# Performance work log

Hardware: AMD Instinct MI355X
Metric: run time of the kernel (lower is better)

The kernel has to match this reference:

```python
import jax, jax.numpy as jnp
import numpy as np

B, L1, Q_DIM, V_DIM = 4, 4096, 256, 256
NH, NL, NP = 8, 4, 4
LEVELS = [(128, 128), (64, 64), (32, 32), (16, 16)]
L2 = sum(h * w for h, w in LEVELS)  # 21760


def setup_inputs() -> dict:
    key = jax.random.key(0)
    ks = jax.random.split(key, 12)
    xav = lambda k, so, si: jax.random.normal(k, (so, si), jnp.float32) * np.sqrt(2.0 / (so + si)).astype(np.float32)
    # reference windows: centers in [0.1,0.9], box sizes in [0.05,0.25]
    c = 0.1 + 0.8 * jax.random.uniform(ks[0], (B, L1, 2), jnp.float32)
    s = 0.05 + 0.2 * jax.random.uniform(ks[1], (B, L1, 2), jnp.float32)
    v_shape = jnp.array(LEVELS, dtype=jnp.int32)
    v_start_index = jnp.array(np.cumsum([0] + [h * w for h, w in LEVELS[:-1]]), dtype=jnp.int32)
    return {
        'query': jax.random.normal(ks[2], (B, L1, Q_DIM), jnp.float32),
        'value': jax.random.normal(ks[3], (B, L2, V_DIM), jnp.float32),
        'v_shape': v_shape,
        'v_mask': jnp.zeros((B, L2), jnp.bool_),
        'v_start_index': v_start_index,
        'v_valid_ratios': jnp.ones((B, 1, 1, NL, 1, 2), jnp.float32),
        'ref_windows': jnp.concatenate([c, s], axis=-1),
        'Wo': 0.01 * jax.random.normal(ks[4], (NH * NL * NP * 2, Q_DIM), jnp.float32),
        'bo': 0.5 * jax.random.normal(ks[5], (NH * NL * NP * 2,), jnp.float32),
        'Wa': 0.02 * jax.random.normal(ks[6], (NH * NL * NP, Q_DIM), jnp.float32),
        'ba': jnp.zeros((NH * NL * NP,), jnp.float32),
        'Wv': xav(ks[7], V_DIM, V_DIM),
        'bv': jnp.zeros((V_DIM,), jnp.float32),
        'Wout': xav(ks[8], Q_DIM, V_DIM),
        'bout': jnp.zeros((Q_DIM,), jnp.float32),
    }


def _ms_deform_sample(value, v_shape, v_start, loc):
    """value: (b,l2,h,d); loc: (b,l1,h,L,P,2) in [0,1] -> (b,l1,L,P,h,d).
    Bilinear sampling with zero padding, align_corners=False semantics."""
    b, l2, h, d = value.shape
    _, l1, _, L, P, _ = loc.shape
    Hi = v_shape[:, 0][None, None, None, :, None]  # (1,1,1,L,1) int
    Wi = v_shape[:, 1][None, None, None, :, None]
    x = loc[..., 0] * Wi.astype(loc.dtype) - 0.5  # (b,l1,h,L,P)
    y = loc[..., 1] * Hi.astype(loc.dtype) - 0.5
    x0 = jnp.floor(x)
    y0 = jnp.floor(y)
    lx, ly = x - x0, y - y0
    x0i = x0.astype(jnp.int32)
    y0i = y0.astype(jnp.int32)
    start = v_start[None, None, None, :, None]
    acc = jnp.zeros((b, l1 * L * P, h, d), loc.dtype)
    for dy, wy in ((0, 1.0 - ly), (1, ly)):
        for dx, wx in ((0, 1.0 - lx), (1, lx)):
            xi = x0i + dx
            yi = y0i + dy
            valid = (xi >= 0) & (xi < Wi) & (yi >= 0) & (yi < Hi)
            w = wx * wy * valid.astype(loc.dtype)  # (b,l1,h,L,P)
            xc = jnp.clip(xi, 0, Wi - 1)
            yc = jnp.clip(yi, 0, Hi - 1)
            flat = start + yc * Wi + xc  # (b,l1,h,L,P) index into l2
            flat_t = flat.transpose(0, 1, 3, 4, 2).reshape(b, l1 * L * P, h)
            w_t = w.transpose(0, 1, 3, 4, 2).reshape(b, l1 * L * P, h)
            g = jnp.take_along_axis(value, flat_t[..., None], axis=1)  # (b,M,h,d)
            acc = acc + g * w_t[..., None]
    return acc.reshape(b, l1, L, P, h, d)


def reference(query, value, v_shape, v_mask, v_start_index, v_valid_ratios, ref_windows,
              Wo, bo, Wa, ba, Wv, bv, Wout, bout):
    b, l1, _ = query.shape
    l2 = value.shape[1]
    hd = value.shape[-1] // NH
    v = value @ Wv.T + bv
    v = jnp.where(v_mask[..., None], 0.0, v).reshape(b, l2, NH, hd)
    off = (query @ Wo.T + bo).reshape(b, l1, NH, NL, NP, 2)
    attn = jax.nn.softmax((query @ Wa.T + ba).reshape(b, l1, NH, NL * NP), axis=-1)
    attn = attn.reshape(b, l1, NH, NL, NP)
    loc = ref_windows[:, :, None, None, None, :2] + off / 8.0 * ref_windows[:, :, None, None, None, 2:]
    loc = loc * v_valid_ratios
    sampled = _ms_deform_sample(v, v_shape, v_start_index, loc)  # (b,l1,L,P,h,d)
    out = jnp.einsum('blLPhd,blhLP->blhd', sampled, attn).reshape(b, l1, NH * hd)
    out = out @ Wout.T + bout
    return out, attn
```

## Files before the change

kernel.cpp:

```cpp
#include <hip/hip_runtime.h>
#include <cstdint>
#include <cstddef>


#define L2_LEN 21760
#define BQ_TOT 16384

typedef __attribute__((ext_vector_type(8))) _Float16 half8;
typedef __attribute__((ext_vector_type(4))) _Float16 half4;
typedef __attribute__((ext_vector_type(2))) _Float16 half2v;
typedef __attribute__((ext_vector_type(4))) float    f32x4;

__device__ __forceinline__ void glds16(const _Float16* g, _Float16* l) {
    __builtin_amdgcn_global_load_lds(
        (const __attribute__((address_space(1))) void*)g,
        (__attribute__((address_space(3))) void*)l, 16, 0, 0);
}
__device__ __forceinline__ half8 cvt8(float4 a, float4 b) {
    half8 h;
    h[0] = (_Float16)a.x; h[1] = (_Float16)a.y;
    h[2] = (_Float16)a.z; h[3] = (_Float16)a.w;
    h[4] = (_Float16)b.x; h[5] = (_Float16)b.y;
    h[6] = (_Float16)b.z; h[7] = (_Float16)b.w;
    return h;
}
__device__ __forceinline__ int swz_chunk(int c) {
    const int frag = c >> 6, r = (c >> 2) & 15, k = c & 3;
    return (frag * 64 + ((k * 16 + r) ^ (k << 2))) * 8;
}

__global__ __launch_bounds__(256, 3) void gemm_vproj(
    const float* __restrict__ A, const float* __restrict__ Wv,
    const float* __restrict__ bv, const unsigned char* __restrict__ mask,
    _Float16* __restrict__ vh)
{
    __shared__ _Float16 As[2][4096];
    __shared__ _Float16 Bs[2][4096];

    const int t = threadIdx.x, lane = t & 63, wid = t >> 6;
    const int wm = wid >> 1, wn = wid & 1;
    const int bm = blockIdx.x, bn = blockIdx.y;

    const int r0 = t >> 2, kg = (t & 3) * 8;
    const float* Ag0 = A  + ((size_t)(bm * 128) + r0) * 256 + kg;
    const float* Ag1 = Ag0 + (size_t)64 * 256;
    const float* Bg0 = Wv + ((size_t)(bn * 128) + r0) * 256 + kg;
    const float* Bg1 = Bg0 + (size_t)64 * 256;
    const int d0 = swz_chunk(t), d1 = swz_chunk(t + 256);
    const int rsw = (lane ^ ((lane >> 4) << 2)) * 8;

    f32x4 acc[4][4] = {};
    float4 pa0, pa1, pa2, pa3, pb0, pb1, pb2, pb3;

    pa0 = *(const float4*)Ag0; pa1 = *(const float4*)(Ag0 + 4);
    pa2 = *(const float4*)Ag1; pa3 = *(const float4*)(Ag1 + 4);
    pb0 = *(const float4*)Bg0; pb1 = *(const float4*)(Bg0 + 4);
    pb2 = *(const float4*)Bg1; pb3 = *(const float4*)(Bg1 + 4);
    *(half8*)&As[0][d0] = cvt8(pa0, pa1); *(half8*)&As[0][d1] = cvt8(pa2, pa3);
    *(half8*)&Bs[0][d0] = cvt8(pb0, pb1); *(half8*)&Bs[0][d1] = cvt8(pb2, pb3);
    __syncthreads();

    for (int it = 0; it < 8; ++it) {
        const int cur = it & 1;
        if (it < 7) {
            const int kk = (it + 1) * 32;
            pa0 = *(const float4*)(Ag0 + kk); pa1 = *(const float4*)(Ag0 + kk + 4);
            pa2 = *(const float4*)(Ag1 + kk); pa3 = *(const float4*)(Ag1 + kk + 4);
            pb0 = *(const float4*)(Bg0 + kk); pb1 = *(const float4*)(Bg0 + kk + 4);
            pb2 = *(const float4*)(Bg1 + kk); pb3 = *(const float4*)(Bg1 + kk + 4);
        }
        half8 ah[4], bh[4];
#pragma unroll
        for (int x = 0; x < 4; ++x) {
            ah[x] = *(const half8*)&As[cur][(wm * 4 + x) * 512 + rsw];
            bh[x] = *(const half8*)&Bs[cur][(wn * 4 + x) * 512 + rsw];
        }
#pragma unroll
        for (int m = 0; m < 4; ++m)
#pragma unroll
            for (int n = 0; n < 4; ++n)
                acc[m][n] = __builtin_amdgcn_mfma_f32_16x16x32_f16(
                    bh[n], ah[m], acc[m][n], 0, 0, 0);
        if (it < 7) {
            *(half8*)&As[cur ^ 1][d0] = cvt8(pa0, pa1);
            *(half8*)&As[cur ^ 1][d1] = cvt8(pa2, pa3);
            *(half8*)&Bs[cur ^ 1][d0] = cvt8(pb0, pb1);
            *(half8*)&Bs[cur ^ 1][d1] = cvt8(pb2, pb3);
        }
        __syncthreads();
    }

    const int cl = lane & 15, rl = (lane >> 4) * 4;
    const int b = bm / 170;
#pragma unroll
    for (int m = 0; m < 4; ++m) {
        const int row = bm * 128 + wm * 64 + m * 16 + cl;
        const float mz = mask[row] ? 0.0f : 1.0f;
        const int l2i = row - b * L2_LEN;
#pragma unroll
        for (int n = 0; n < 4; ++n) {
            const int col = bn * 128 + wn * 64 + n * 16 + rl;
            const float4 bb = *(const float4*)(bv + col);
            const int h = col >> 5, c = col & 31;
            half4 o;
            o[0] = (_Float16)((acc[m][n][0] + bb.x) * mz);
            o[1] = (_Float16)((acc[m][n][1] + bb.y) * mz);
            o[2] = (_Float16)((acc[m][n][2] + bb.z) * mz);
            o[3] = (_Float16)((acc[m][n][3] + bb.w) * mz);
            *(half4*)(vh + ((size_t)(b * 8 + h) * L2_LEN + l2i) * 32 + c) = o;
        }
    }
}

template<bool A_F16>
__global__ __launch_bounds__(256, 3) void gemm_qo(
    const void* __restrict__ Av,
    const float* __restrict__ W0, const float* __restrict__ W1,
    const float* __restrict__ b0, const float* __restrict__ b1, int n_split,
    float* __restrict__ C, int ldC)
{
    __shared__ _Float16 As[2][4096];
    __shared__ _Float16 Bs[2][4096];

    const int t = threadIdx.x, lane = t & 63, wid = t >> 6;
    const int wm = wid >> 1, wn = wid & 1;
    const int bm = blockIdx.x, bn = blockIdx.y;

    const int cb = bn * 128;
    const float* Wt; const float* bt;
    if (cb < n_split) { Wt = W0 + (size_t)cb * 256;             bt = b0 + cb; }
    else              { Wt = W1 + (size_t)(cb - n_split) * 256; bt = b1 + (cb - n_split); }

    const int r0 = t >> 2, kg = (t & 3) * 8;
    const float* Bg0 = Wt + ((size_t)r0) * 256 + kg;
    const float* Bg1 = Bg0 + (size_t)64 * 256;
    const int d0 = swz_chunk(t), d1 = swz_chunk(t + 256);
    const int rsw = (lane ^ ((lane >> 4) << 2)) * 8;

    const float* Agf0 = nullptr; const float* Agf1 = nullptr;
    const _Float16* Agh0 = nullptr; const _Float16* Agh1 = nullptr;
    _Float16* AdH0 = nullptr; _Float16* AdH1 = nullptr;
    if (A_F16) {
        const int u0 = wid * 128 + lane, u1 = u0 + 64;
        const int ar0 = ((u0 >> 6) << 4) + (u0 & 15), ak0 = ((u0 >> 4) & 3) * 8;
        const int ar1 = ((u1 >> 6) << 4) + (u1 & 15), ak1 = ((u1 >> 4) & 3) * 8;
        Agh0 = (const _Float16*)Av + ((size_t)(bm * 128) + ar0) * 256 + ak0;
        Agh1 = (const _Float16*)Av + ((size_t)(bm * 128) + ar1) * 256 + ak1;
        AdH0 = (_Float16*)&As[0][0] + wid * 1024;
        AdH1 = AdH0 + 512;
    } else {
        Agf0 = (const float*)Av + ((size_t)(bm * 128) + r0) * 256 + kg;
        Agf1 = Agf0 + (size_t)64 * 256;
    }

    f32x4 acc[4][4] = {};
    float4 pa0, pa1, pa2, pa3, pb0, pb1, pb2, pb3;

    pb0 = *(const float4*)Bg0; pb1 = *(const float4*)(Bg0 + 4);
    pb2 = *(const float4*)Bg1; pb3 = *(const float4*)(Bg1 + 4);
    if (A_F16) { glds16(Agh0, AdH0); glds16(Agh1, AdH1); }
    else {
        pa0 = *(const float4*)Agf0; pa1 = *(const float4*)(Agf0 + 4);
        pa2 = *(const float4*)Agf1; pa3 = *(const float4*)(Agf1 + 4);
        *(half8*)&As[0][d0] = cvt8(pa0, pa1);
        *(half8*)&As[0][d1] = cvt8(pa2, pa3);
    }
    *(half8*)&Bs[0][d0] = cvt8(pb0, pb1);
    *(half8*)&Bs[0][d1] = cvt8(pb2, pb3);
    __syncthreads();

    for (int it = 0; it < 8; ++it) {
        const int cur = it & 1;
        if (it < 7) {
            const int kk = (it + 1) * 32;
            if (A_F16) {
                glds16(Agh0 + kk, AdH0 + (cur ^ 1) * 4096);
                glds16(Agh1 + kk, AdH1 + (cur ^ 1) * 4096);
            } else {
                pa0 = *(const float4*)(Agf0 + kk); pa1 = *(const float4*)(Agf0 + kk + 4);
                pa2 = *(const float4*)(Agf1 + kk); pa3 = *(const float4*)(Agf1 + kk + 4);
            }
            pb0 = *(const float4*)(Bg0 + kk); pb1 = *(const float4*)(Bg0 + kk + 4);
            pb2 = *(const float4*)(Bg1 + kk); pb3 = *(const float4*)(Bg1 + kk + 4);
        }
        half8 ah[4], bh[4];
#pragma unroll
        for (int x = 0; x < 4; ++x) {
            ah[x] = *(const half8*)&As[cur][(wm * 4 + x) * 512 + (A_F16 ? lane * 8 : rsw)];
            bh[x] = *(const half8*)&Bs[cur][(wn * 4 + x) * 512 + rsw];
        }
#pragma unroll
        for (int m = 0; m < 4; ++m)
#pragma unroll
            for (int n = 0; n < 4; ++n)
                acc[m][n] = __builtin_amdgcn_mfma_f32_16x16x32_f16(
                    bh[n], ah[m], acc[m][n], 0, 0, 0);
        if (it < 7) {
            if (!A_F16) {
                *(half8*)&As[cur ^ 1][d0] = cvt8(pa0, pa1);
                *(half8*)&As[cur ^ 1][d1] = cvt8(pa2, pa3);
            }
            *(half8*)&Bs[cur ^ 1][d0] = cvt8(pb0, pb1);
            *(half8*)&Bs[cur ^ 1][d1] = cvt8(pb2, pb3);
        }
        __syncthreads();
    }

    const int cl = lane & 15, rl = (lane >> 4) * 4;
#pragma unroll
    for (int m = 0; m < 4; ++m) {
        const int row = bm * 128 + wm * 64 + m * 16 + cl;
#pragma unroll
        for (int n = 0; n < 4; ++n) {
            const int co = wn * 64 + n * 16 + rl;
            const float4 bb = *(const float4*)(bt + co);
            float4 r;
            r.x = acc[m][n][0] + bb.x; r.y = acc[m][n][1] + bb.y;
            r.z = acc[m][n][2] + bb.z; r.w = acc[m][n][3] + bb.w;
            *(float4*)(C + (size_t)row * ldC + cb + co) = r;
        }
    }
}

__global__ __launch_bounds__(128) void sample_fused(
    const _Float16* __restrict__ v,
    const float* __restrict__ qp,
    const float* __restrict__ ref,
    const float* __restrict__ vrp,
    float* __restrict__ attn_out,
    _Float16* __restrict__ sout)
{
    const int t  = threadIdx.x;
    const int q  = blockIdx.x * 4 + (t >> 5);
    const int h  = (t >> 2) & 7;
    const int lv = t & 3;
    const int b  = q >> 12;

    const float* lg = qp + (size_t)q * 384 + 256 + h * 16;
    const float4 l0 = ((const float4*)lg)[0], l1 = ((const float4*)lg)[1];
    const float4 l2 = ((const float4*)lg)[2], l3 = ((const float4*)lg)[3];
    float e[16] = {l0.x, l0.y, l0.z, l0.w, l1.x, l1.y, l1.z, l1.w,
                   l2.x, l2.y, l2.z, l2.w, l3.x, l3.y, l3.z, l3.w};
    float mx = e[0];
#pragma unroll
    for (int j = 1; j < 16; ++j) mx = fmaxf(mx, e[j]);
    float sum = 0.0f;
#pragma unroll
    for (int j = 0; j < 16; ++j) { e[j] = __expf(e[j] - mx); sum += e[j]; }
    const float inv = 1.0f / sum;
    float aw[4];
#pragma unroll
    for (int p = 0; p < 4; ++p) aw[p] = e[lv * 4 + p] * inv;
    *(float4*)(attn_out + ((size_t)q * 8 + h) * 16 + lv * 4) =
        make_float4(aw[0], aw[1], aw[2], aw[3]);

    const float4 rw = *(const float4*)(ref + (size_t)q * 4);
    const float* op = qp + (size_t)q * 384 + h * 32 + lv * 8;
    const float4 o01 = ((const float4*)op)[0], o23 = ((const float4*)op)[1];
    const float oxv[4] = {o01.x, o01.z, o23.x, o23.z};
    const float oyv[4] = {o01.y, o01.w, o23.y, o23.w};

    const int HW = 128 >> lv;
    constexpr int SS[4] = {0, 16384, 20480, 21504};
    const int start = SS[0] * 0 + (lv == 0 ? 0 : (lv == 1 ? 16384 : (lv == 2 ? 20480 : 21504)));
    const float fHW = (float)HW;
    const float vrx = vrp[(b * 4 + lv) * 2 + 0];
    const float vry = vrp[(b * 4 + lv) * 2 + 1];
    const _Float16* vb = v + ((size_t)(b * 8 + h) * L2_LEN + start) * 32;

    float acc[32] = {};

#pragma unroll
    for (int p = 0; p < 4; ++p) {
        const float a = aw[p];
        const float x = (rw.x + oxv[p] * 0.125f * rw.z) * vrx * fHW - 0.5f;
        const float y = (rw.y + oyv[p] * 0.125f * rw.w) * vry * fHW - 0.5f;
        const float x0f = floorf(x), y0f = floorf(y);
        const float fx = x - x0f, fy = y - y0f;
        const int x0 = (int)x0f, y0 = (int)y0f;
        const float wx0 = (x0 >= 0 && x0 < HW)         ? (1.0f - fx) : 0.0f;
        const float wx1 = (x0 + 1 >= 0 && x0 + 1 < HW) ? fx          : 0.0f;
        const float wy0 = (y0 >= 0 && y0 < HW)         ? (1.0f - fy) : 0.0f;
        const float wy1 = (y0 + 1 >= 0 && y0 + 1 < HW) ? fy          : 0.0f;
        const int xc0 = min(max(x0, 0), HW - 1), xc1 = min(max(x0 + 1, 0), HW - 1);
        const int yc0 = min(max(y0, 0), HW - 1), yc1 = min(max(y0 + 1, 0), HW - 1);
        half2v wA, wB;
        wA[0] = (_Float16)(wx0 * wy0 * a); wA[1] = (_Float16)(wx1 * wy0 * a);
        wB[0] = (_Float16)(wx0 * wy1 * a); wB[1] = (_Float16)(wx1 * wy1 * a);

        const uint4* p00 = (const uint4*)(vb + (size_t)(yc0 * HW + xc0) * 32);
        const uint4* p01 = (const uint4*)(vb + (size_t)(yc0 * HW + xc1) * 32);
        const uint4* p10 = (const uint4*)(vb + (size_t)(yc1 * HW + xc0) * 32);
        const uint4* p11 = (const uint4*)(vb + (size_t)(yc1 * HW + xc1) * 32);
        unsigned u00[16], u01[16], u10[16], u11[16];
#pragma unroll
        for (int i = 0; i < 4; ++i) {
            *(uint4*)&u00[i * 4] = p00[i];
            *(uint4*)&u01[i * 4] = p01[i];
            *(uint4*)&u10[i * 4] = p10[i];
            *(uint4*)&u11[i * 4] = p11[i];
        }
#pragma unroll
        for (int d = 0; d < 16; ++d) {
            const unsigned loA = __builtin_amdgcn_perm(u00[d], u01[d], 0x01000504u);
            const unsigned hiA = __builtin_amdgcn_perm(u00[d], u01[d], 0x03020706u);
            const unsigned loB = __builtin_amdgcn_perm(u10[d], u11[d], 0x01000504u);
            const unsigned hiB = __builtin_amdgcn_perm(u10[d], u11[d], 0x03020706u);
#if __has_builtin(__builtin_amdgcn_fdot2)
            acc[2 * d]     = __builtin_amdgcn_fdot2(__builtin_bit_cast(half2v, loA), wA, acc[2 * d], false);
            acc[2 * d]     = __builtin_amdgcn_fdot2(__builtin_bit_cast(half2v, loB), wB, acc[2 * d], false);
            acc[2 * d + 1] = __builtin_amdgcn_fdot2(__builtin_bit_cast(half2v, hiA), wA, acc[2 * d + 1], false);
            acc[2 * d + 1] = __builtin_amdgcn_fdot2(__builtin_bit_cast(half2v, hiB), wB, acc[2 * d + 1], false);
#else
            const half2v xA = __builtin_bit_cast(half2v, loA), yA = __builtin_bit_cast(half2v, hiA);
            const half2v xB = __builtin_bit_cast(half2v, loB), yB = __builtin_bit_cast(half2v, hiB);
            acc[2 * d]     += (float)xA[0] * (float)wA[0] + (float)xA[1] * (float)wA[1]
                            + (float)xB[0] * (float)wB[0] + (float)xB[1] * (float)wB[1];
            acc[2 * d + 1] += (float)yA[0] * (float)wA[0] + (float)yA[1] * (float)wA[1]
                            + (float)yB[0] * (float)wB[0] + (float)yB[1] * (float)wB[1];
#endif
        }
    }

    float t1[32];
#pragma unroll
    for (int j = 0; j < 32; ++j) t1[j] = __shfl_xor(acc[j], 1);
    float r16[16];
#pragma unroll
    for (int j = 0; j < 16; ++j)
        r16[j] = (lv & 1) ? (acc[16 + j] + t1[16 + j]) : (acc[j] + t1[j]);
    float t2[16];
#pragma unroll
    for (int j = 0; j < 16; ++j) t2[j] = __shfl_xor(r16[j], 2);
    float r8[8];
#pragma unroll
    for (int j = 0; j < 8; ++j)
        r8[j] = (lv & 2) ? (r16[8 + j] + t2[8 + j]) : (r16[j] + t2[j]);

    const int cq = ((lv & 1) << 4) | ((lv & 2) << 2);
    half8 o;
#pragma unroll
    for (int j = 0; j < 8; ++j) o[j] = (_Float16)r8[j];
    *(half8*)(sout + (size_t)q * 256 + h * 32 + cq) = o;
}

extern "C" void kernel_launch(void* const* d_in, const int* in_sizes, int n_in,
                              void* d_out, int out_size, void* d_ws, size_t ws_size,
                              hipStream_t stream)
{
    const float*         query    = (const float*)d_in[0];
    const float*         value    = (const float*)d_in[1];
    const unsigned char* v_mask   = (const unsigned char*)d_in[3];
    const float*         v_ratios = (const float*)d_in[5];
    const float*         ref_w    = (const float*)d_in[6];
    const float*         Wo       = (const float*)d_in[7];
    const float*         bo       = (const float*)d_in[8];
    const float*         Wa       = (const float*)d_in[9];
    const float*         ba       = (const float*)d_in[10];
    const float*         Wv       = (const float*)d_in[11];
    const float*         bv       = (const float*)d_in[12];
    const float*         Wout     = (const float*)d_in[13];
    const float*         bout     = (const float*)d_in[14];

    float* out      = (float*)d_out;
    float* attn_out = out + (size_t)BQ_TOT * 256;

    float*    qp = (float*)d_ws;
    _Float16* vh = (_Float16*)(qp + (size_t)BQ_TOT * 384);
    _Float16* Sf = vh + (size_t)4 * L2_LEN * 256;

    gemm_vproj<<<dim3(680, 2), 256, 0, stream>>>(value, Wv, bv, v_mask, vh);
    gemm_qo<false><<<dim3(128, 3), 256, 0, stream>>>(
        query, Wo, Wa, bo, ba, 256, qp, 384);
    sample_fused<<<4096, 128, 0, stream>>>(vh, qp, ref_w, v_ratios, attn_out, Sf);
    gemm_qo<true><<<dim3(128, 2), 256, 0, stream>>>(
        Sf, Wout, Wout, bout, bout, 256, out, 256);
}
```

Baseline: 309.9 us.

## Widen vproj tile to full N and split sampling lanes by channel

```diff
diff --git a/kernel.cpp b/kernel.cpp
--- a/kernel.cpp
+++ b/kernel.cpp
@@ -29,43 +29,41 @@
     return (frag * 64 + ((k * 16 + r) ^ (k << 2))) * 8;
 }
 
-__global__ __launch_bounds__(256, 3) void gemm_vproj(
+__global__ __launch_bounds__(512) void gemm_vproj(
     const float* __restrict__ A, const float* __restrict__ Wv,
     const float* __restrict__ bv, const unsigned char* __restrict__ mask,
     _Float16* __restrict__ vh)
 {
     __shared__ _Float16 As[2][4096];
-    __shared__ _Float16 Bs[2][4096];
+    __shared__ _Float16 Bs[2][8192];
 
     const int t = threadIdx.x, lane = t & 63, wid = t >> 6;
-    const int wm = wid >> 1, wn = wid & 1;
-    const int bm = blockIdx.x, bn = blockIdx.y;
-
-    const int r0 = t >> 2, kg = (t & 3) * 8;
-    const float* Ag0 = A  + ((size_t)(bm * 128) + r0) * 256 + kg;
-    const float* Ag1 = Ag0 + (size_t)64 * 256;
-    const float* Bg0 = Wv + ((size_t)(bn * 128) + r0) * 256 + kg;
-    const float* Bg1 = Bg0 + (size_t)64 * 256;
-    const int d0 = swz_chunk(t), d1 = swz_chunk(t + 256);
+    const int wm = wid >> 2, wn = wid & 3;
+    const int bm = blockIdx.x;
+
+    const float* Ag = A + ((size_t)(bm * 128) + (t >> 2)) * 256 + (t & 3) * 8;
+    const int da = swz_chunk(t);
+    const float* Bg0 = Wv + ((size_t)(t >> 2)) * 256 + (t & 3) * 8;
+    const float* Bg1 = Bg0 + (size_t)128 * 256;
+    const int db0 = swz_chunk(t), db1 = swz_chunk(t + 512);
     const int rsw = (lane ^ ((lane >> 4) << 2)) * 8;
 
     f32x4 acc[4][4] = {};
-    float4 pa0, pa1, pa2, pa3, pb0, pb1, pb2, pb3;
-
-    pa0 = *(const float4*)Ag0; pa1 = *(const float4*)(Ag0 + 4);
-    pa2 = *(const float4*)Ag1; pa3 = *(const float4*)(Ag1 + 4);
+    float4 pa0, pa1, pb0, pb1, pb2, pb3;
+
+    pa0 = *(const float4*)Ag;  pa1 = *(const float4*)(Ag + 4);
     pb0 = *(const float4*)Bg0; pb1 = *(const float4*)(Bg0 + 4);
     pb2 = *(const float4*)Bg1; pb3 = *(const float4*)(Bg1 + 4);
-    *(half8*)&As[0][d0] = cvt8(pa0, pa1); *(half8*)&As[0][d1] = cvt8(pa2, pa3);
-    *(half8*)&Bs[0][d0] = cvt8(pb0, pb1); *(half8*)&Bs[0][d1] = cvt8(pb2, pb3);
+    *(half8*)&As[0][da]  = cvt8(pa0, pa1);
+    *(half8*)&Bs[0][db0] = cvt8(pb0, pb1);
+    *(half8*)&Bs[0][db1] = cvt8(pb2, pb3);
     __syncthreads();
 
     for (int it = 0; it < 8; ++it) {
         const int cur = it & 1;
         if (it < 7) {
             const int kk = (it + 1) * 32;
-            pa0 = *(const float4*)(Ag0 + kk); pa1 = *(const float4*)(Ag0 + kk + 4);
-            pa2 = *(const float4*)(Ag1 + kk); pa3 = *(const float4*)(Ag1 + kk + 4);
+            pa0 = *(const float4*)(Ag + kk);  pa1 = *(const float4*)(Ag + kk + 4);
             pb0 = *(const float4*)(Bg0 + kk); pb1 = *(const float4*)(Bg0 + kk + 4);
             pb2 = *(const float4*)(Bg1 + kk); pb3 = *(const float4*)(Bg1 + kk + 4);
         }
@@ -82,10 +80,9 @@
                 acc[m][n] = __builtin_amdgcn_mfma_f32_16x16x32_f16(
                     bh[n], ah[m], acc[m][n], 0, 0, 0);
         if (it < 7) {
-            *(half8*)&As[cur ^ 1][d0] = cvt8(pa0, pa1);
-            *(half8*)&As[cur ^ 1][d1] = cvt8(pa2, pa3);
-            *(half8*)&Bs[cur ^ 1][d0] = cvt8(pb0, pb1);
-            *(half8*)&Bs[cur ^ 1][d1] = cvt8(pb2, pb3);
+            *(half8*)&As[cur ^ 1][da]  = cvt8(pa0, pa1);
+            *(half8*)&Bs[cur ^ 1][db0] = cvt8(pb0, pb1);
+            *(half8*)&Bs[cur ^ 1][db1] = cvt8(pb2, pb3);
         }
         __syncthreads();
     }
@@ -99,7 +96,7 @@
         const int l2i = row - b * L2_LEN;
 #pragma unroll
         for (int n = 0; n < 4; ++n) {
-            const int col = bn * 128 + wn * 64 + n * 16 + rl;
+            const int col = wn * 64 + n * 16 + rl;
             const float4 bb = *(const float4*)(bv + col);
             const int h = col >> 5, c = col & 31;
             half4 o;
@@ -233,115 +230,103 @@
     const int t  = threadIdx.x;
     const int q  = blockIdx.x * 4 + (t >> 5);
     const int h  = (t >> 2) & 7;
-    const int lv = t & 3;
+    const int c0 = (t & 3) * 8;
     const int b  = q >> 12;
 
     const float* lg = qp + (size_t)q * 384 + 256 + h * 16;
     const float4 l0 = ((const float4*)lg)[0], l1 = ((const float4*)lg)[1];
     const float4 l2 = ((const float4*)lg)[2], l3 = ((const float4*)lg)[3];
-    float e[16] = {l0.x, l0.y, l0.z, l0.w, l1.x, l1.y, l1.z, l1.w,
-                   l2.x, l2.y, l2.z, l2.w, l3.x, l3.y, l3.z, l3.w};
-    float mx = e[0];
-#pragma unroll
-    for (int j = 1; j < 16; ++j) mx = fmaxf(mx, e[j]);
+    float aw[16] = {l0.x, l0.y, l0.z, l0.w, l1.x, l1.y, l1.z, l1.w,
+                    l2.x, l2.y, l2.z, l2.w, l3.x, l3.y, l3.z, l3.w};
+    float mx = aw[0];
+#pragma unroll
+    for (int j = 1; j < 16; ++j) mx = fmaxf(mx, aw[j]);
     float sum = 0.0f;
 #pragma unroll
-    for (int j = 0; j < 16; ++j) { e[j] = __expf(e[j] - mx); sum += e[j]; }
+    for (int j = 0; j < 16; ++j) { aw[j] = __expf(aw[j] - mx); sum += aw[j]; }
     const float inv = 1.0f / sum;
-    float aw[4];
-#pragma unroll
-    for (int p = 0; p < 4; ++p) aw[p] = e[lv * 4 + p] * inv;
-    *(float4*)(attn_out + ((size_t)q * 8 + h) * 16 + lv * 4) =
-        make_float4(aw[0], aw[1], aw[2], aw[3]);
-
+#pragma unroll
+    for (int j = 0; j < 16; ++j) aw[j] *= inv;
+    if (c0 == 0) {
+        float4* ao = (float4*)(attn_out + ((size_t)q * 8 + h) * 16);
+        ao[0] = make_float4(aw[0], aw[1], aw[2], aw[3]);
+        ao[1] = make_float4(aw[4], aw[5], aw[6], aw[7]);
+        ao[2] = make_float4(aw[8], aw[9], aw[10], aw[11]);
+        ao[3] = make_float4(aw[12], aw[13], aw[14], aw[15]);
+    }
+
+    const float* op = qp + (size_t)q * 384 + h * 32;
+    float4 of[8];
+#pragma unroll
+    for (int i = 0; i < 8; ++i) of[i] = ((const float4*)op)[i];
     const float4 rw = *(const float4*)(ref + (size_t)q * 4);
-    const float* op = qp + (size_t)q * 384 + h * 32 + lv * 8;
-    const float4 o01 = ((const float4*)op)[0], o23 = ((const float4*)op)[1];
-    const float oxv[4] = {o01.x, o01.z, o23.x, o23.z};
-    const float oyv[4] = {o01.y, o01.w, o23.y, o23.w};
-
-    const int HW = 128 >> lv;
+    const float4 vr01 = ((const float4*)(vrp + b * 8))[0];
+    const float4 vr23 = ((const float4*)(vrp + b * 8))[1];
+
+    const _Float16* vbase = v + ((size_t)(b * 8 + h) * L2_LEN) * 32 + c0;
     constexpr int SS[4] = {0, 16384, 20480, 21504};
-    const int start = SS[0] * 0 + (lv == 0 ? 0 : (lv == 1 ? 16384 : (lv == 2 ? 20480 : 21504)));
-    const float fHW = (float)HW;
-    const float vrx = vrp[(b * 4 + lv) * 2 + 0];
-    const float vry = vrp[(b * 4 + lv) * 2 + 1];
-    const _Float16* vb = v + ((size_t)(b * 8 + h) * L2_LEN + start) * 32;
-
-    float acc[32] = {};
-
-#pragma unroll
-    for (int p = 0; p < 4; ++p) {
-        const float a = aw[p];
-        const float x = (rw.x + oxv[p] * 0.125f * rw.z) * vrx * fHW - 0.5f;
-        const float y = (rw.y + oyv[p] * 0.125f * rw.w) * vry * fHW - 0.5f;
-        const float x0f = floorf(x), y0f = floorf(y);
-        const float fx = x - x0f, fy = y - y0f;
-        const int x0 = (int)x0f, y0 = (int)y0f;
-        const float wx0 = (x0 >= 0 && x0 < HW)         ? (1.0f - fx) : 0.0f;
-        const float wx1 = (x0 + 1 >= 0 && x0 + 1 < HW) ? fx          : 0.0f;
-        const float wy0 = (y0 >= 0 && y0 < HW)         ? (1.0f - fy) : 0.0f;
-        const float wy1 = (y0 + 1 >= 0 && y0 + 1 < HW) ? fy          : 0.0f;
-        const int xc0 = min(max(x0, 0), HW - 1), xc1 = min(max(x0 + 1, 0), HW - 1);
-        const int yc0 = min(max(y0, 0), HW - 1), yc1 = min(max(y0 + 1, 0), HW - 1);
-        half2v wA, wB;
-        wA[0] = (_Float16)(wx0 * wy0 * a); wA[1] = (_Float16)(wx1 * wy0 * a);
-        wB[0] = (_Float16)(wx0 * wy1 * a); wB[1] = (_Float16)(wx1 * wy1 * a);
-
-        const uint4* p00 = (const uint4*)(vb + (size_t)(yc0 * HW + xc0) * 32);
-        const uint4* p01 = (const uint4*)(vb + (size_t)(yc0 * HW + xc1) * 32);
-        const uint4* p10 = (const uint4*)(vb + (size_t)(yc1 * HW + xc0) * 32);
-        const uint4* p11 = (const uint4*)(vb + (size_t)(yc1 * HW + xc1) * 32);
-        unsigned u00[16], u01[16], u10[16], u11[16];
-#pragma unroll
-        for (int i = 0; i < 4; ++i) {
-            *(uint4*)&u00[i * 4] = p00[i];
-            *(uint4*)&u01[i * 4] = p01[i];
-            *(uint4*)&u10[i * 4] = p10[i];
-            *(uint4*)&u11[i * 4] = p11[i];
-        }
-#pragma unroll
-        for (int d = 0; d < 16; ++d) {
-            const unsigned loA = __builtin_amdgcn_perm(u00[d], u01[d], 0x01000504u);
-            const unsigned hiA = __builtin_amdgcn_perm(u00[d], u01[d], 0x03020706u);
-            const unsigned loB = __builtin_amdgcn_perm(u10[d], u11[d], 0x01000504u);
-            const unsigned hiB = __builtin_amdgcn_perm(u10[d], u11[d], 0x03020706u);
-#if __has_builtin(__builtin_amdgcn_fdot2)
-            acc[2 * d]     = __builtin_amdgcn_fdot2(__builtin_bit_cast(half2v, loA), wA, acc[2 * d], false);
-            acc[2 * d]     = __builtin_amdgcn_fdot2(__builtin_bit_cast(half2v, loB), wB, acc[2 * d], false);
-            acc[2 * d + 1] = __builtin_amdgcn_fdot2(__builtin_bit_cast(half2v, hiA), wA, acc[2 * d + 1], false);
-            acc[2 * d + 1] = __builtin_amdgcn_fdot2(__builtin_bit_cast(half2v, hiB), wB, acc[2 * d + 1], false);
-#else
-            const half2v xA = __builtin_bit_cast(half2v, loA), yA = __builtin_bit_cast(half2v, hiA);
-            const half2v xB = __builtin_bit_cast(half2v, loB), yB = __builtin_bit_cast(half2v, hiB);
-            acc[2 * d]     += (float)xA[0] * (float)wA[0] + (float)xA[1] * (float)wA[1]
-                            + (float)xB[0] * (float)wB[0] + (float)xB[1] * (float)wB[1];
-            acc[2 * d + 1] += (float)yA[0] * (float)wA[0] + (float)yA[1] * (float)wA[1]
-                            + (float)yB[0] * (float)wB[0] + (float)yB[1] * (float)wB[1];
-#endif
-        }
-    }
-
-    float t1[32];
-#pragma unroll
-    for (int j = 0; j < 32; ++j) t1[j] = __shfl_xor(acc[j], 1);
-    float r16[16];
-#pragma unroll
-    for (int j = 0; j < 16; ++j)
-        r16[j] = (lv & 1) ? (acc[16 + j] + t1[16 + j]) : (acc[j] + t1[j]);
-    float t2[16];
-#pragma unroll
-    for (int j = 0; j < 16; ++j) t2[j] = __shfl_xor(r16[j], 2);
-    float r8[8];
-#pragma unroll
-    for (int j = 0; j < 8; ++j)
-        r8[j] = (lv & 2) ? (r16[8 + j] + t2[8 + j]) : (r16[j] + t2[j]);
-
-    const int cq = ((lv & 1) << 4) | ((lv & 2) << 2);
+
+    float acc[8] = {};
+
+#pragma unroll
+    for (int l = 0; l < 4; ++l) {
+        const int HW = 128 >> l;
+        const float fHW = (float)HW;
+        const float vrx = (l == 0) ? vr01.x : (l == 1) ? vr01.z : (l == 2) ? vr23.x : vr23.z;
+        const float vry = (l == 0) ? vr01.y : (l == 1) ? vr01.w : (l == 2) ? vr23.y : vr23.w;
+        const _Float16* vb = vbase + (size_t)SS[l] * 32;
+
+        uint4  g[16];
+        half2v wA[4], wB[4];
+#pragma unroll
+        for (int p = 0; p < 4; ++p) {
+            const int pt = l * 4 + p;
+            const float4 o4 = of[pt >> 1];
+            const float ox = (pt & 1) ? o4.z : o4.x;
+            const float oy = (pt & 1) ? o4.w : o4.y;
+            const float a  = aw[pt];
+            const float x = (rw.x + ox * 0.125f * rw.z) * vrx * fHW - 0.5f;
+            const float y = (rw.y + oy * 0.125f * rw.w) * vry * fHW - 0.5f;
+            const float x0f = floorf(x), y0f = floorf(y);
+            const float fx = x - x0f, fy = y - y0f;
+            const int x0 = (int)x0f, y0 = (int)y0f;
+            const float wx0 = (x0 >= 0 && x0 < HW)         ? (1.0f - fx) : 0.0f;
+            const float wx1 = (x0 + 1 >= 0 && x0 + 1 < HW) ? fx          : 0.0f;
+            const float wy0 = (y0 >= 0 && y0 < HW)         ? (1.0f - fy) : 0.0f;
+            const float wy1 = (y0 + 1 >= 0 && y0 + 1 < HW) ? fy          : 0.0f;
+            const int xc0 = min(max(x0, 0), HW - 1), xc1 = min(max(x0 + 1, 0), HW - 1);
+            const int yc0 = min(max(y0, 0), HW - 1), yc1 = min(max(y0 + 1, 0), HW - 1);
+            wA[p][0] = (_Float16)(wx0 * wy0 * a); wA[p][1] = (_Float16)(wx1 * wy0 * a);
+            wB[p][0] = (_Float16)(wx0 * wy1 * a); wB[p][1] = (_Float16)(wx1 * wy1 * a);
+            g[p * 4 + 0] = *(const uint4*)(vb + (size_t)(yc0 * HW + xc0) * 32);
+            g[p * 4 + 1] = *(const uint4*)(vb + (size_t)(yc0 * HW + xc1) * 32);
+            g[p * 4 + 2] = *(const uint4*)(vb + (size_t)(yc1 * HW + xc0) * 32);
+            g[p * 4 + 3] = *(const uint4*)(vb + (size_t)(yc1 * HW + xc1) * 32);
+        }
+#pragma unroll
+        for (int p = 0; p < 4; ++p) {
+            const uint4 t00 = g[p * 4 + 0], t01 = g[p * 4 + 1];
+            const uint4 t10 = g[p * 4 + 2], t11 = g[p * 4 + 3];
+#pragma unroll
+            for (int d = 0; d < 4; ++d) {
+                const unsigned a0 = (&t00.x)[d], a1 = (&t01.x)[d];
+                const unsigned b0_ = (&t10.x)[d], b1_ = (&t11.x)[d];
+                const unsigned loA = __builtin_amdgcn_perm(a0, a1, 0x01000504u);
+                const unsigned hiA = __builtin_amdgcn_perm(a0, a1, 0x03020706u);
+                const unsigned loB = __builtin_amdgcn_perm(b0_, b1_, 0x01000504u);
+                const unsigned hiB = __builtin_amdgcn_perm(b0_, b1_, 0x03020706u);
+                acc[2 * d]     = __builtin_amdgcn_fdot2(__builtin_bit_cast(half2v, loA), wA[p], acc[2 * d],     false);
+                acc[2 * d]     = __builtin_amdgcn_fdot2(__builtin_bit_cast(half2v, loB), wB[p], acc[2 * d],     false);
+                acc[2 * d + 1] = __builtin_amdgcn_fdot2(__builtin_bit_cast(half2v, hiA), wA[p], acc[2 * d + 1], false);
+                acc[2 * d + 1] = __builtin_amdgcn_fdot2(__builtin_bit_cast(half2v, hiB), wB[p], acc[2 * d + 1], false);
+            }
+        }
+    }
+
     half8 o;
 #pragma unroll
-    for (int j = 0; j < 8; ++j) o[j] = (_Float16)r8[j];
-    *(half8*)(sout + (size_t)q * 256 + h * 32 + cq) = o;
+    for (int j = 0; j < 8; ++j) o[j] = (_Float16)acc[j];
+    *(half8*)(sout + (size_t)q * 256 + h * 32 + c0) = o;
 }
 
 extern "C" void kernel_launch(void* const* d_in, const int* in_sizes, int n_in,
@@ -369,7 +354,7 @@
     _Float16* vh = (_Float16*)(qp + (size_t)BQ_TOT * 384);
     _Float16* Sf = vh + (size_t)4 * L2_LEN * 256;
 
-    gemm_vproj<<<dim3(680, 2), 256, 0, stream>>>(value, Wv, bv, v_mask, vh);
+    gemm_vproj<<<680, 512, 0, stream>>>(value, Wv, bv, v_mask, vh);
     gemm_qo<false><<<dim3(128, 3), 256, 0, stream>>>(
         query, Wo, Wa, bo, ba, 256, qp, 384);
     sample_fused<<<4096, 128, 0, stream>>>(vh, qp, ref_w, v_ratios, attn_out, Sf);
```

Result: faster. 276.5 us (-10.8%).
